# Kernel tuning notes

Measured on AMD Instinct MI355X. Metric: run time of the kernel, lower is better.

The kernel has to match this reference:

```python
import jax, jax.numpy as jnp
import numpy as np

ALPHA = 0.2      # GAT leaky_relu slope (args.alpha)
MLP_SLOPE = 0.01 # F.leaky_relu default in the MLP path
NEG = -9e15

def _l2_normalize(x, axis=1, eps=1e-12):
    n = jnp.sqrt(jnp.sum(x * x, axis=axis, keepdims=True))
    return x / jnp.maximum(n, eps)

def setup_inputs() -> dict:
    key = jax.random.key(0)
    ks = jax.random.split(key, 14)
    N, Din, Dh, H, Dg, M1, M2, E = 8192, 512, 256, 2, 512, 512, 256, 100000
    x = jax.random.normal(ks[0], (N, Din), dtype=jnp.float32)
    adj = jax.random.randint(ks[1], (N, N), 0, 2, dtype=jnp.int32)
    train_sample = jax.random.randint(ks[2], (E, 2), 0, N, dtype=jnp.int32)
    llm_emb = jax.random.normal(ks[3], (N, Dg), dtype=jnp.float32)
    # GAT head params (stacked over heads)
    Wg = jax.random.normal(ks[4], (H, Din, Dh), dtype=jnp.float32) * 0.05
    a1 = jax.random.normal(ks[5], (H, Dh), dtype=jnp.float32) * 0.05
    a2 = jax.random.normal(ks[6], (H, Dh), dtype=jnp.float32) * 0.05
    bias_g = jnp.zeros((H, Dh), dtype=jnp.float32)
    # MLP params
    W1 = jax.random.normal(ks[7], (Dh + Dg, M1), dtype=jnp.float32) * 0.03
    b1 = jnp.zeros((M1,), dtype=jnp.float32)
    W2 = jax.random.normal(ks[8], (M1, M2), dtype=jnp.float32) * 0.04
    b2 = jnp.zeros((M2,), dtype=jnp.float32)
    return {"x": x, "adj": adj, "train_sample": train_sample, "llm_emb": llm_emb,
            "Wg": Wg, "a1": a1, "a2": a2, "bias_g": bias_g,
            "W1": W1, "b1": b1, "W2": W2, "b2": b2}

def reference(x, adj, train_sample, llm_emb, Wg, a1, a2, bias_g, W1, b1, W2, b2):
    mask = adj > 0  # [N, N]

    def head(W, av1, av2, b):
        h = x @ W                                   # [N, Dh]
        s1 = h @ av1                                # [N]
        s2 = h @ av2                                # [N]
        e = jax.nn.leaky_relu(s1[:, None] + s2[None, :], ALPHA)  # [N, N]
        att = jax.nn.softmax(jnp.where(mask, e, NEG), axis=1)
        out = att @ h                               # [N, Dh]
        out = jax.nn.leaky_relu(out, ALPHA)
        out = _l2_normalize(out, axis=1)
        return out + b

    # encode: single GNN layer -> mean over heads (dropout inactive in eval)
    out_heads = jax.vmap(head)(Wg, a1, a2, bias_g)  # [H, N, Dh]
    embed_gnn = jnp.mean(out_heads, axis=0)         # [N, Dh]
    embed = jnp.concatenate([llm_emb, embed_gnn], axis=1)  # [N, Dg+Dh]

    def mlp(z):
        z = jax.nn.leaky_relu(z @ W1 + b1, MLP_SLOPE)
        z = jax.nn.leaky_relu(z @ W2 + b2, MLP_SLOPE)
        return z

    tf_embed = mlp(embed)
    target_embed = mlp(embed)
    train_tf = tf_embed[train_sample[:, 0]]
    train_tg = target_embed[train_sample[:, 1]]
    pred = jnp.sum(train_tf * train_tg, axis=1, keepdims=True)  # dot decode, [E,1]
    return pred
```

## Files before the change

kernel.cpp:

```cpp
#include <hip/hip_runtime.h>
#include <hip/hip_bf16.h>
#include <cstdint>
#include <cstddef>

#define ALPHA 0.2f
#define MLP_SLOPE 0.01f

typedef short bf16x8 __attribute__((ext_vector_type(8)));
typedef float f32x4 __attribute__((ext_vector_type(4)));
typedef unsigned short ushort_t;

#define ASM_BARRIER() __asm__ __volatile__("s_waitcnt lgkmcnt(0)\n\ts_barrier" ::: "memory")

__device__ __forceinline__ float lrelu(float x, float s) { return x > 0.f ? x : x * s; }
__device__ __forceinline__ ushort_t f2bf(float x) {
  __hip_bfloat16 h = __float2bfloat16(x);
  return *reinterpret_cast<ushort_t*>(&h);
}
__device__ __forceinline__ float bf2f(ushort_t u) {
  union { unsigned int i; float f; } v; v.i = ((unsigned int)u) << 16; return v.f;
}

__global__ __launch_bounds__(256) void split_f(
    const float* __restrict__ in, ushort_t* __restrict__ hi,
    ushort_t* __restrict__ lo)
{
  int idx = blockIdx.x * 256 + threadIdx.x;
  float4 v = ((const float4*)in)[idx];
  ushort4 h, l;
  h.x = f2bf(v.x); l.x = f2bf(v.x - bf2f(h.x));
  h.y = f2bf(v.y); l.y = f2bf(v.y - bf2f(h.y));
  h.z = f2bf(v.z); l.z = f2bf(v.z - bf2f(h.z));
  h.w = f2bf(v.w); l.w = f2bf(v.w - bf2f(h.w));
  ((ushort4*)hi)[idx] = h;
  ((ushort4*)lo)[idx] = l;
}

__global__ __launch_bounds__(256) void pack_wt(
    const float* __restrict__ W, ushort_t* __restrict__ hi,
    ushort_t* __restrict__ lo, int K, int N)
{
  int gid = blockIdx.x * 256 + threadIdx.x;
  int lane = gid & 63;
  int kbc = K >> 5;
  int kblk = (gid >> 6) % kbc;
  int nblk = (gid >> 6) / kbc;
  size_t b = (size_t)blockIdx.y * K * N;
  int col = nblk * 16 + (lane & 15);
  int krow = kblk * 32 + (lane >> 4) * 8;
  ushort_t h[8] __attribute__((aligned(16)));
  ushort_t l[8] __attribute__((aligned(16)));
#pragma unroll
  for (int e = 0; e < 8; ++e) {
    float v = W[b + (size_t)(krow + e) * N + col];
    h[e] = f2bf(v);
    l[e] = f2bf(v - bf2f(h[e]));
  }
  *(uint4*)&hi[b + (size_t)gid * 8] = *(uint4*)h;
  *(uint4*)&lo[b + (size_t)gid * 8] = *(uint4*)l;
}

__global__ __launch_bounds__(256) void gemm_nolds(
    const ushort_t* __restrict__ Ahi, const ushort_t* __restrict__ Alo,
    const ushort_t* __restrict__ Bph, const ushort_t* __restrict__ Bpl,
    const float* __restrict__ bias, float* __restrict__ Cf,
    ushort_t* __restrict__ Chi, ushort_t* __restrict__ Clo,
    int M, int N, int K, float slope, int act)
{
  const size_t boff = (size_t)blockIdx.z * N * K;
  const size_t coff = (size_t)blockIdx.z * M * N;
  const int t = threadIdx.x;
  const int wave = t >> 6, l63 = t & 63;
  const int l16 = t & 15, oct = (t >> 4) & 3, quad = oct;
  const int wm = (wave & 1) * 64, wn = (wave >> 1) * 32;
  const int m0 = blockIdx.y * 128 + wm;
  const int nb = blockIdx.x * 4 + (wave >> 1) * 2;
  const int nbase = blockIdx.x * 64 + wn;
  const int ksteps = K >> 5;

  const ushort_t* aph[4];
  const ushort_t* apl[4];
#pragma unroll
  for (int mt = 0; mt < 4; ++mt) {
    size_t o = (size_t)(m0 + mt * 16 + l16) * K + oct * 8;
    aph[mt] = Ahi + o;
    apl[mt] = Alo + o;
  }
  const ushort_t* bph[2];
  const ushort_t* bpl[2];
#pragma unroll
  for (int nt = 0; nt < 2; ++nt) {
    size_t o = boff + ((size_t)(nb + nt) * ksteps * 64 + l63) * 8;
    bph[nt] = Bph + o;
    bpl[nt] = Bpl + o;
  }

  f32x4 acc[4][2];
#pragma unroll
  for (int i = 0; i < 4; ++i)
#pragma unroll
    for (int j = 0; j < 2; ++j) acc[i][j] = (f32x4){0.f, 0.f, 0.f, 0.f};

#define LOADF(AH, AL, BH, BL, KB)                                         \
  {                                                                       \
    _Pragma("unroll") for (int mt = 0; mt < 4; ++mt) {                    \
      AH[mt] = *(const bf16x8*)(aph[mt] + (size_t)(KB) * 32);             \
      AL[mt] = *(const bf16x8*)(apl[mt] + (size_t)(KB) * 32);             \
    }                                                                     \
    _Pragma("unroll") for (int nt = 0; nt < 2; ++nt) {                    \
      BH[nt] = *(const bf16x8*)(bph[nt] + (size_t)(KB) * 512);            \
      BL[nt] = *(const bf16x8*)(bpl[nt] + (size_t)(KB) * 512);            \
    }                                                                     \
  }
#define MF(AH, AL, BH, BL)                                                \
  {                                                                       \
    _Pragma("unroll") for (int mt = 0; mt < 4; ++mt)                      \
    _Pragma("unroll") for (int nt = 0; nt < 2; ++nt) {                    \
      acc[mt][nt] = __builtin_amdgcn_mfma_f32_16x16x32_bf16(AH[mt], BH[nt], acc[mt][nt], 0, 0, 0); \
      acc[mt][nt] = __builtin_amdgcn_mfma_f32_16x16x32_bf16(AH[mt], BL[nt], acc[mt][nt], 0, 0, 0); \
      acc[mt][nt] = __builtin_amdgcn_mfma_f32_16x16x32_bf16(AL[mt], BH[nt], acc[mt][nt], 0, 0, 0); \
    }                                                                     \
  }

  bf16x8 ah0[4], al0[4], bh0[2], bl0[2];
  bf16x8 ah1[4], al1[4], bh1[2], bl1[2];
  LOADF(ah0, al0, bh0, bl0, 0)
  for (int kb = 0; kb < ksteps; kb += 2) {
    LOADF(ah1, al1, bh1, bl1, kb + 1)
    MF(ah0, al0, bh0, bl0)
    if (kb + 2 < ksteps) LOADF(ah0, al0, bh0, bl0, kb + 2)
    MF(ah1, al1, bh1, bl1)
  }
#undef LOADF
#undef MF

#pragma unroll
  for (int mt = 0; mt < 4; ++mt)
#pragma unroll
    for (int nt = 0; nt < 2; ++nt)
#pragma unroll
      for (int rg = 0; rg < 4; ++rg) {
        int m = m0 + mt * 16 + quad * 4 + rg;
        int n = nbase + nt * 16 + l16;
        float v = acc[mt][nt][rg];
        if (bias) v += bias[n];
        if (act) v = lrelu(v, slope);
        size_t o = coff + (size_t)m * N + n;
        if (Cf) Cf[o] = v;
        if (Chi) {
          ushort_t h = f2bf(v);
          Chi[o] = h; Clo[o] = f2bf(v - bf2f(h));
        }
      }
}

__global__ __launch_bounds__(256) void s_kernel(
    const float* __restrict__ hbuf, const float* __restrict__ a1,
    const float* __restrict__ a2, float* __restrict__ s1, float* __restrict__ s2)
{
  const int gw = (blockIdx.x * 256 + threadIdx.x) >> 6;
  const int lane = threadIdx.x & 63;
#pragma unroll
  for (int hh = 0; hh < 2; ++hh) {
    float4 hv = ((const float4*)(hbuf + ((size_t)hh * 8192 + gw) * 256))[lane];
    float4 a1v = ((const float4*)(a1 + hh * 256))[lane];
    float4 a2v = ((const float4*)(a2 + hh * 256))[lane];
    float p1 = hv.x * a1v.x + hv.y * a1v.y + hv.z * a1v.z + hv.w * a1v.w;
    float p2 = hv.x * a2v.x + hv.y * a2v.y + hv.z * a2v.z + hv.w * a2v.w;
    for (int off = 32; off > 0; off >>= 1) {
      p1 += __shfl_xor(p1, off);
      p2 += __shfl_xor(p2, off);
    }
    if (lane == 0) {
      s1[hh * 8192 + gw] = p1;
      s2[hh * 8192 + gw] = p2;
    }
  }
}

__global__ __launch_bounds__(256) void h_pack(
    const float* __restrict__ hbuf, ushort_t* __restrict__ Bpack)
{
  int gid = blockIdx.x * 256 + threadIdx.x;
  int lane = gid & 63;
  int ntile = (gid >> 6) & 15;
  int kblk = (gid >> 10) & 255;
  int head = gid >> 18;
  int c = ntile * 16 + (lane & 15);
  int jb = kblk * 32 + (lane >> 4) * 8;
  ushort_t o[8] __attribute__((aligned(16)));
#pragma unroll
  for (int e = 0; e < 8; ++e)
    o[e] = f2bf(hbuf[((size_t)head * 8192 + jb + e) * 256 + c]);
  *(uint4*)&Bpack[(size_t)gid * 8] = *(uint4*)o;
}

__global__ __launch_bounds__(256, 2) void attn_mfma6(
    const ushort_t* __restrict__ Bpack, const float* __restrict__ s1g,
    const float* __restrict__ s2g, const int* __restrict__ adj,
    ushort_t* __restrict__ pacc, float* __restrict__ pl)
{
  __shared__ ushort_t Wlds[2][2][4][64][8];
  const int t = threadIdx.x;
  const int i0 = blockIdx.x * 64;
  const int js = blockIdx.y;
  const int kbase = js * 2048;
  const int wr = t >> 2, kq = t & 3;
  const int glane = kq * 16 + (wr & 15);
  const int gmt = wr >> 4;
  const float s1v0 = s1g[i0 + wr];
  const float s1v1 = s1g[8192 + i0 + wr];
  const int wave = t >> 6, head = wave >> 1, nh = wave & 1;
  const int l16 = t & 15, quad = (t >> 4) & 3;
  const int l63 = t & 63;
  f32x4 acc[4][8];
#pragma unroll
  for (int m = 0; m < 4; ++m)
#pragma unroll
    for (int n = 0; n < 8; ++n) acc[m][n] = (f32x4){0.f, 0.f, 0.f, 0.f};
  float rs0 = 0.f, rs1 = 0.f;

  const int* arow = adj + (size_t)(i0 + wr) * 8192;
  int4 pa0, pa1;
  float4 p20a, p20b, p21a, p21b;

  auto fetch = [&](int kk) {
    pa0 = *(const int4*)&arow[kk];
    pa1 = *(const int4*)&arow[kk + 4];
    p20a = *(const float4*)&s2g[kk];
    p20b = *(const float4*)&s2g[kk + 4];
    p21a = *(const float4*)&s2g[8192 + kk];
    p21b = *(const float4*)&s2g[8192 + kk + 4];
  };
  auto gen = [&](int buf) {
    int am[8] = {pa0.x, pa0.y, pa0.z, pa0.w, pa1.x, pa1.y, pa1.z, pa1.w};
    float s20[8] = {p20a.x, p20a.y, p20a.z, p20a.w, p20b.x, p20b.y, p20b.z, p20b.w};
    float s21[8] = {p21a.x, p21a.y, p21a.z, p21a.w, p21b.x, p21b.y, p21b.z, p21b.w};
    ushort_t w0[8] __attribute__((aligned(16)));
    ushort_t w1[8] __attribute__((aligned(16)));
#pragma unroll
    for (int e = 0; e < 8; ++e) {
      float e0 = s1v0 + s20[e];
      float e1 = s1v1 + s21[e];
      e0 = fmaxf(e0, 0.f) + ALPHA * fminf(e0, 0.f);
      e1 = fmaxf(e1, 0.f) + ALPHA * fminf(e1, 0.f);
      float v0 = am[e] > 0 ? __expf(e0) : 0.f;
      float v1 = am[e] > 0 ? __expf(e1) : 0.f;
      rs0 += v0; rs1 += v1;
      w0[e] = f2bf(v0); w1[e] = f2bf(v1);
    }
    *(uint4*)&Wlds[buf][0][gmt][glane][0] = *(uint4*)w0;
    *(uint4*)&Wlds[buf][1][gmt][glane][0] = *(uint4*)w1;
  };

  fetch(kbase + kq * 8);
  gen(0);
  fetch(kbase + 32 + kq * 8);
  ASM_BARRIER();

  for (int kt = 0; kt < 64; ++kt) {
    const int cur = kt & 1, nxt = cur ^ 1;
    const int kblk = js * 64 + kt;
    const ushort_t* bb =
        Bpack + ((((size_t)head * 256 + kblk) * 16 + nh * 8) * 64 + l63) * 8;
    bf16x8 Bf[8];
#pragma unroll
    for (int nt = 0; nt < 8; ++nt)
      Bf[nt] = *(const bf16x8*)&bb[nt * 512];
    bf16x8 Af[4];
#pragma unroll
    for (int mt = 0; mt < 4; ++mt)
      Af[mt] = *(const bf16x8*)&Wlds[cur][head][mt][l63][0];
#pragma unroll
    for (int mt = 0; mt < 4; ++mt)
#pragma unroll
      for (int nt = 0; nt < 8; ++nt)
        acc[mt][nt] = __builtin_amdgcn_mfma_f32_16x16x32_bf16(
            Af[mt], Bf[nt], acc[mt][nt], 0, 0, 0);
    if (kt < 63) {
      gen(nxt);
      if (kt < 62) fetch(kbase + (kt + 2) * 32 + kq * 8);
    }
    ASM_BARRIER();
  }

  rs0 += __shfl_xor(rs0, 1); rs0 += __shfl_xor(rs0, 2);
  rs1 += __shfl_xor(rs1, 1); rs1 += __shfl_xor(rs1, 2);
  if (kq == 0) {
    pl[((size_t)js * 2 + 0) * 8192 + i0 + wr] = rs0;
    pl[((size_t)js * 2 + 1) * 8192 + i0 + wr] = rs1;
  }
  const int n0 = nh * 128;
#pragma unroll
  for (int mt = 0; mt < 4; ++mt)
#pragma unroll
    for (int nt = 0; nt < 8; ++nt)
#pragma unroll
      for (int rg = 0; rg < 4; ++rg) {
        int row = i0 + mt * 16 + quad * 4 + rg;
        int col = n0 + nt * 16 + l16;
        pacc[(((size_t)js * 2 + head) * 8192 + row) * 256 + col] =
            f2bf(acc[mt][nt][rg]);
      }
}

__global__ __launch_bounds__(256) void attn_finalize(
    const ushort_t* __restrict__ pacc, const float* __restrict__ pl,
    const float* __restrict__ bg, const float* __restrict__ llm,
    float* __restrict__ embed)
{
  __shared__ float red[8];
  const int r = blockIdx.x;
  const int t = threadIdx.x;
  const int wv = t >> 6, lane = t & 63;
  if (t < 128)
    *(float4*)&embed[(size_t)r * 768 + t * 4] =
        *(const float4*)&llm[(size_t)r * 512 + t * 4];
  float o[2];
#pragma unroll
  for (int hh = 0; hh < 2; ++hh) {
    float num = 0.f, l = 0.f;
#pragma unroll
    for (int js = 0; js < 4; ++js) {
      num += bf2f(pacc[(((size_t)js * 2 + hh) * 8192 + r) * 256 + t]);
      l += pl[((size_t)js * 2 + hh) * 8192 + r];
    }
    o[hh] = lrelu(num / l, ALPHA);
  }
  float v0 = o[0] * o[0], v1 = o[1] * o[1];
  for (int off = 32; off > 0; off >>= 1) {
    v0 += __shfl_xor(v0, off);
    v1 += __shfl_xor(v1, off);
  }
  if (lane == 0) { red[wv] = v0; red[4 + wv] = v1; }
  __syncthreads();
  float n0 = fmaxf(sqrtf(red[0] + red[1] + red[2] + red[3]), 1e-12f);
  float n1 = fmaxf(sqrtf(red[4] + red[5] + red[6] + red[7]), 1e-12f);
  embed[(size_t)r * 768 + 512 + t] =
      0.5f * (o[0] / n0 + bg[t] + o[1] / n1 + bg[256 + t]);
}

__global__ __launch_bounds__(256) void pred_kernel(
    const float* __restrict__ z2, const int* __restrict__ ts,
    float* __restrict__ out, int E)
{
  const int gw = (blockIdx.x * 256 + threadIdx.x) >> 6;
  const int lane = threadIdx.x & 63;
  if (gw >= E) return;
  const int a = ts[gw * 2], b = ts[gw * 2 + 1];
  float4 va = ((const float4*)(z2 + (size_t)a * 256))[lane];
  float4 vb = ((const float4*)(z2 + (size_t)b * 256))[lane];
  float p = va.x * vb.x + va.y * vb.y + va.z * vb.z + va.w * vb.w;
  for (int off = 32; off > 0; off >>= 1) p += __shfl_xor(p, off);
  if (lane == 0) out[gw] = p;
}

extern "C" void kernel_launch(void* const* d_in, const int* in_sizes, int n_in,
                              void* d_out, int out_size, void* d_ws, size_t ws_size,
                              hipStream_t stream) {
  const float* x   = (const float*)d_in[0];
  const int*   adj = (const int*)d_in[1];
  const int*   ts  = (const int*)d_in[2];
  const float* llm = (const float*)d_in[3];
  const float* Wg  = (const float*)d_in[4];
  const float* a1  = (const float*)d_in[5];
  const float* a2  = (const float*)d_in[6];
  const float* bg  = (const float*)d_in[7];
  const float* W1  = (const float*)d_in[8];
  const float* b1  = (const float*)d_in[9];
  const float* W2  = (const float*)d_in[10];
  const float* b2  = (const float*)d_in[11];
  float* out = (float*)d_out;
  float* ws  = (float*)d_ws;
  const int E = in_sizes[2] / 2;

  float*    hbuf  = ws;
  ushort_t* Bpack = (ushort_t*)(ws + 4194304);
  float*    embed = ws;
  ushort_t* xhi   = (ushort_t*)(ws + 6291456);
  ushort_t* xlo   = (ushort_t*)(ws + 8388608);
  ushort_t* z1hi  = xhi;
  ushort_t* z1lo  = xlo;
  float*    s1    = ws + 10485760;
  float*    s2    = ws + 10502144;
  float*    pl    = ws + 10518528;
  ushort_t* pacc  = (ushort_t*)(ws + 10584064);
  ushort_t* ehi   = (ushort_t*)(ws + 10584064);
  ushort_t* elo   = (ushort_t*)(ws + 13729792);
  float*    z2    = ws + 16875520;
  ushort_t* wgphi = (ushort_t*)(ws + 18972672);
  ushort_t* wgplo = (ushort_t*)(ws + 19103744);
  ushort_t* w1phi = (ushort_t*)(ws + 19234816);
  ushort_t* w1plo = (ushort_t*)(ws + 19431424);
  ushort_t* w2phi = (ushort_t*)(ws + 19628032);
  ushort_t* w2plo = (ushort_t*)(ws + 19693568);

  split_f<<<4096, 256, 0, stream>>>(x, xhi, xlo);
  pack_wt<<<dim3(64, 2), 256, 0, stream>>>(Wg, wgphi, wgplo, 512, 256);
  pack_wt<<<dim3(192, 1), 256, 0, stream>>>(W1, w1phi, w1plo, 768, 512);
  pack_wt<<<dim3(64, 1), 256, 0, stream>>>(W2, w2phi, w2plo, 512, 256);
  gemm_nolds<<<dim3(4, 64, 2), 256, 0, stream>>>(
      xhi, xlo, wgphi, wgplo, nullptr, hbuf, nullptr, nullptr,
      8192, 256, 512, 0.f, 0);
  s_kernel<<<2048, 256, 0, stream>>>(hbuf, a1, a2, s1, s2);
  h_pack<<<2048, 256, 0, stream>>>(hbuf, Bpack);
  attn_mfma6<<<dim3(128, 4), 256, 0, stream>>>(Bpack, s1, s2, adj, pacc, pl);
  attn_finalize<<<8192, 256, 0, stream>>>(pacc, pl, bg, llm, embed);
  split_f<<<6144, 256, 0, stream>>>(embed, ehi, elo);
  gemm_nolds<<<dim3(8, 64, 1), 256, 0, stream>>>(
      ehi, elo, w1phi, w1plo, b1, nullptr, z1hi, z1lo,
      8192, 512, 768, MLP_SLOPE, 1);
  gemm_nolds<<<dim3(4, 64, 1), 256, 0, stream>>>(
      z1hi, z1lo, w2phi, w2plo, b2, z2, nullptr, nullptr,
      8192, 256, 512, MLP_SLOPE, 1);
  pred_kernel<<<(E * 64 + 255) / 256, 256, 0, stream>>>(z2, ts, out, E);
}
```

Baseline: 658.7 us.

## Shrink attention row tile to 32 rows and split heads across threads

The attention kernel now processes 32 query rows per block instead of 64, doubling the grid. The weight-generation work is split so each thread handles one head instead of both, and launch bounds rise to 3 blocks per SM. This cuts accumulator registers and per-thread exp work to raise occupancy and parallelism. The cost is that each Bpack tile is loaded for half as many rows, doubling B-operand global traffic per output and lowering the MFMA-to-load ratio.

Result: slower. 750.7 us (+14.0%).

```diff
diff --git a/kernel.cpp b/kernel.cpp
--- a/kernel.cpp
+++ b/kernel.cpp
@@ -195,62 +195,56 @@
   *(uint4*)&Bpack[(size_t)gid * 8] = *(uint4*)o;
 }
 
-__global__ __launch_bounds__(256, 2) void attn_mfma6(
+__global__ __launch_bounds__(256, 3) void attn_mfma7(
     const ushort_t* __restrict__ Bpack, const float* __restrict__ s1g,
     const float* __restrict__ s2g, const int* __restrict__ adj,
     ushort_t* __restrict__ pacc, float* __restrict__ pl)
 {
-  __shared__ ushort_t Wlds[2][2][4][64][8];
+  __shared__ ushort_t Wlds[2][2][2][64][8];
   const int t = threadIdx.x;
-  const int i0 = blockIdx.x * 64;
+  const int i0 = blockIdx.x * 32;
   const int js = blockIdx.y;
   const int kbase = js * 2048;
-  const int wr = t >> 2, kq = t & 3;
+  const int wr = t >> 3;
+  const int ghead = (t >> 2) & 1;
+  const int kq = t & 3;
   const int glane = kq * 16 + (wr & 15);
   const int gmt = wr >> 4;
-  const float s1v0 = s1g[i0 + wr];
-  const float s1v1 = s1g[8192 + i0 + wr];
+  const float s1v = s1g[(size_t)ghead * 8192 + i0 + wr];
+  const float* s2h = s2g + (size_t)ghead * 8192;
+  const int* arow = adj + (size_t)(i0 + wr) * 8192;
   const int wave = t >> 6, head = wave >> 1, nh = wave & 1;
   const int l16 = t & 15, quad = (t >> 4) & 3;
   const int l63 = t & 63;
-  f32x4 acc[4][8];
-#pragma unroll
-  for (int m = 0; m < 4; ++m)
+  f32x4 acc[2][8];
+#pragma unroll
+  for (int m = 0; m < 2; ++m)
 #pragma unroll
     for (int n = 0; n < 8; ++n) acc[m][n] = (f32x4){0.f, 0.f, 0.f, 0.f};
-  float rs0 = 0.f, rs1 = 0.f;
-
-  const int* arow = adj + (size_t)(i0 + wr) * 8192;
+  float rs = 0.f;
+
   int4 pa0, pa1;
-  float4 p20a, p20b, p21a, p21b;
-
+  float4 ps2a, ps2b;
   auto fetch = [&](int kk) {
     pa0 = *(const int4*)&arow[kk];
     pa1 = *(const int4*)&arow[kk + 4];
-    p20a = *(const float4*)&s2g[kk];
-    p20b = *(const float4*)&s2g[kk + 4];
-    p21a = *(const float4*)&s2g[8192 + kk];
-    p21b = *(const float4*)&s2g[8192 + kk + 4];
+    ps2a = *(const float4*)&s2h[kk];
+    ps2b = *(const float4*)&s2h[kk + 4];
   };
   auto gen = [&](int buf) {
     int am[8] = {pa0.x, pa0.y, pa0.z, pa0.w, pa1.x, pa1.y, pa1.z, pa1.w};
-    float s20[8] = {p20a.x, p20a.y, p20a.z, p20a.w, p20b.x, p20b.y, p20b.z, p20b.w};
-    float s21[8] = {p21a.x, p21a.y, p21a.z, p21a.w, p21b.x, p21b.y, p21b.z, p21b.w};
-    ushort_t w0[8] __attribute__((aligned(16)));
-    ushort_t w1[8] __attribute__((aligned(16)));
+    float s2v[8] = {ps2a.x, ps2a.y, ps2a.z, ps2a.w,
+                    ps2b.x, ps2b.y, ps2b.z, ps2b.w};
+    ushort_t w[8] __attribute__((aligned(16)));
 #pragma unroll
     for (int e = 0; e < 8; ++e) {
-      float e0 = s1v0 + s20[e];
-      float e1 = s1v1 + s21[e];
-      e0 = fmaxf(e0, 0.f) + ALPHA * fminf(e0, 0.f);
-      e1 = fmaxf(e1, 0.f) + ALPHA * fminf(e1, 0.f);
-      float v0 = am[e] > 0 ? __expf(e0) : 0.f;
-      float v1 = am[e] > 0 ? __expf(e1) : 0.f;
-      rs0 += v0; rs1 += v1;
-      w0[e] = f2bf(v0); w1[e] = f2bf(v1);
+      float ev = s1v + s2v[e];
+      ev = fmaxf(ev, 0.f) + ALPHA * fminf(ev, 0.f);
+      float wv = am[e] > 0 ? __expf(ev) : 0.f;
+      rs += wv;
+      w[e] = f2bf(wv);
     }
-    *(uint4*)&Wlds[buf][0][gmt][glane][0] = *(uint4*)w0;
-    *(uint4*)&Wlds[buf][1][gmt][glane][0] = *(uint4*)w1;
+    *(uint4*)&Wlds[buf][ghead][gmt][glane][0] = *(uint4*)w;
   };
 
   fetch(kbase + kq * 8);
@@ -267,12 +261,12 @@
 #pragma unroll
     for (int nt = 0; nt < 8; ++nt)
       Bf[nt] = *(const bf16x8*)&bb[nt * 512];
-    bf16x8 Af[4];
-#pragma unroll
-    for (int mt = 0; mt < 4; ++mt)
+    bf16x8 Af[2];
+#pragma unroll
+    for (int mt = 0; mt < 2; ++mt)
       Af[mt] = *(const bf16x8*)&Wlds[cur][head][mt][l63][0];
 #pragma unroll
-    for (int mt = 0; mt < 4; ++mt)
+    for (int mt = 0; mt < 2; ++mt)
 #pragma unroll
       for (int nt = 0; nt < 8; ++nt)
         acc[mt][nt] = __builtin_amdgcn_mfma_f32_16x16x32_bf16(
@@ -284,15 +278,13 @@
     ASM_BARRIER();
   }
 
-  rs0 += __shfl_xor(rs0, 1); rs0 += __shfl_xor(rs0, 2);
-  rs1 += __shfl_xor(rs1, 1); rs1 += __shfl_xor(rs1, 2);
-  if (kq == 0) {
-    pl[((size_t)js * 2 + 0) * 8192 + i0 + wr] = rs0;
-    pl[((size_t)js * 2 + 1) * 8192 + i0 + wr] = rs1;
-  }
+  rs += __shfl_xor(rs, 1); rs += __shfl_xor(rs, 2);
+  if (kq == 0)
+    pl[((size_t)js * 2 + ghead) * 8192 + i0 + wr] = rs;
+
   const int n0 = nh * 128;
 #pragma unroll
-  for (int mt = 0; mt < 4; ++mt)
+  for (int mt = 0; mt < 2; ++mt)
 #pragma unroll
     for (int nt = 0; nt < 8; ++nt)
 #pragma unroll
@@ -404,7 +396,7 @@
       8192, 256, 512, 0.f, 0);
   s_kernel<<<2048, 256, 0, stream>>>(hbuf, a1, a2, s1, s2);
   h_pack<<<2048, 256, 0, stream>>>(hbuf, Bpack);
-  attn_mfma6<<<dim3(128, 4), 256, 0, stream>>>(Bpack, s1, s2, adj, pacc, pl);
+  attn_mfma7<<<dim3(256, 4), 256, 0, stream>>>(Bpack, s1, s2, adj, pacc, pl);
   attn_finalize<<<8192, 256, 0, stream>>>(pacc, pl, bg, llm, embed);
   split_f<<<6144, 256, 0, stream>>>(embed, ehi, elo);
   gemm_nolds<<<dim3(8, 64, 1), 256, 0, stream>>>(
```

## Fuse GAT projection with score/pack epilogue, single-bf16 x, LDS-staged GEMMs

Applied to the files above, without the earlier changes.

The x@Wg projection now uses a single bf16 pass instead of the hi/lo split. Its epilogue writes the packed bf16 B-operand for attention directly and accumulates s1/s2 with atomics, which removes the fp32 hbuf round trip and the separate s_kernel and h_pack launches. attn_finalize writes the split bf16 embedding directly, so the separate split pass is gone. The MLP GEMMs stage A tiles through double-buffered LDS. Dropping the lo term for x and h lowers precision, and the atomics make the s1/s2 summation order nondeterministic.

Result: faster. 594.5 us (-9.8%).

```diff
diff --git a/kernel.cpp b/kernel.cpp
--- a/kernel.cpp
+++ b/kernel.cpp
@@ -21,19 +21,20 @@
   union { unsigned int i; float f; } v; v.i = ((unsigned int)u) << 16; return v.f;
 }
 
-__global__ __launch_bounds__(256) void split_f(
-    const float* __restrict__ in, ushort_t* __restrict__ hi,
-    ushort_t* __restrict__ lo)
+__global__ __launch_bounds__(256) void tobf(
+    const float* __restrict__ in, ushort_t* __restrict__ outp)
 {
   int idx = blockIdx.x * 256 + threadIdx.x;
   float4 v = ((const float4*)in)[idx];
-  ushort4 h, l;
-  h.x = f2bf(v.x); l.x = f2bf(v.x - bf2f(h.x));
-  h.y = f2bf(v.y); l.y = f2bf(v.y - bf2f(h.y));
-  h.z = f2bf(v.z); l.z = f2bf(v.z - bf2f(h.z));
-  h.w = f2bf(v.w); l.w = f2bf(v.w - bf2f(h.w));
-  ((ushort4*)hi)[idx] = h;
-  ((ushort4*)lo)[idx] = l;
+  ushort4 h;
+  h.x = f2bf(v.x); h.y = f2bf(v.y); h.z = f2bf(v.z); h.w = f2bf(v.w);
+  ((ushort4*)outp)[idx] = h;
+}
+
+__global__ __launch_bounds__(256) void zero_f(float* __restrict__ p)
+{
+  int idx = blockIdx.x * 256 + threadIdx.x;
+  ((float4*)p)[idx] = make_float4(0.f, 0.f, 0.f, 0.f);
 }
 
 __global__ __launch_bounds__(256) void pack_wt(
@@ -57,43 +58,127 @@
     l[e] = f2bf(v - bf2f(h[e]));
   }
   *(uint4*)&hi[b + (size_t)gid * 8] = *(uint4*)h;
-  *(uint4*)&lo[b + (size_t)gid * 8] = *(uint4*)l;
-}
-
-__global__ __launch_bounds__(256) void gemm_nolds(
+  if (lo) *(uint4*)&lo[b + (size_t)gid * 8] = *(uint4*)l;
+}
+
+__global__ __launch_bounds__(256, 2) void gemm_h(
+    const ushort_t* __restrict__ xb, const ushort_t* __restrict__ Wgp,
+    const float* __restrict__ a1, const float* __restrict__ a2,
+    ushort_t* __restrict__ Bpack, float* __restrict__ s1,
+    float* __restrict__ s2)
+{
+  __shared__ ushort_t Ab[2][128][40];
+  const int t = threadIdx.x;
+  const int head = blockIdx.z;
+  const int m0 = blockIdx.y * 128;
+  const int n0 = blockIdx.x * 64;
+  const int wave = t >> 6;
+  const int wm = (wave & 1) * 64, wn = (wave >> 1) * 32;
+  const int l16 = t & 15, quad = (t >> 4) & 3, l63 = t & 63;
+  const int sr = t >> 1, sp = (t & 1) * 16;
+  const ushort_t* arow_g = xb + (size_t)(m0 + sr) * 512 + sp;
+  const ushort_t* bp = Wgp + (size_t)head * 256 * 512;
+  const int nb0 = (n0 + wn) >> 4;
+
+  f32x4 acc[4][2];
+#pragma unroll
+  for (int i = 0; i < 4; ++i)
+#pragma unroll
+    for (int j = 0; j < 2; ++j) acc[i][j] = (f32x4){0.f, 0.f, 0.f, 0.f};
+
+  uint4 r0, r1;
+  r0 = *(const uint4*)(arow_g);
+  r1 = *(const uint4*)(arow_g + 8);
+  *(uint4*)&Ab[0][sr][sp] = r0;
+  *(uint4*)&Ab[0][sr][sp + 8] = r1;
+  __syncthreads();
+
+  for (int kb = 0; kb < 16; ++kb) {
+    const int cur = kb & 1, nxt = cur ^ 1;
+    if (kb < 15) {
+      const ushort_t* p = arow_g + (kb + 1) * 32;
+      r0 = *(const uint4*)p;
+      r1 = *(const uint4*)(p + 8);
+    }
+    bf16x8 Bf[2];
+#pragma unroll
+    for (int nt = 0; nt < 2; ++nt)
+      Bf[nt] = *(const bf16x8*)&bp[(((size_t)(nb0 + nt) * 16 + kb) * 64 + l63) * 8];
+    bf16x8 Af[4];
+#pragma unroll
+    for (int mt = 0; mt < 4; ++mt)
+      Af[mt] = *(const bf16x8*)&Ab[cur][wm + mt * 16 + l16][quad * 8];
+#pragma unroll
+    for (int mt = 0; mt < 4; ++mt)
+#pragma unroll
+      for (int nt = 0; nt < 2; ++nt)
+        acc[mt][nt] = __builtin_amdgcn_mfma_f32_16x16x32_bf16(
+            Af[mt], Bf[nt], acc[mt][nt], 0, 0, 0);
+    if (kb < 15) {
+      *(uint4*)&Ab[nxt][sr][sp] = r0;
+      *(uint4*)&Ab[nxt][sr][sp + 8] = r1;
+    }
+    __syncthreads();
+  }
+
+#pragma unroll
+  for (int mt = 0; mt < 4; ++mt)
+#pragma unroll
+    for (int nt = 0; nt < 2; ++nt)
+#pragma unroll
+      for (int rg = 0; rg < 4; ++rg) {
+        int j = m0 + wm + mt * 16 + quad * 4 + rg;
+        int c = n0 + wn + nt * 16 + l16;
+        int kblk = j >> 5;
+        int laneb = ((j >> 3) & 3) * 16 + (c & 15);
+        int e = j & 7;
+        Bpack[(((size_t)head * 256 + kblk) * 16 + (c >> 4)) * 512 + laneb * 8 + e] =
+            f2bf(acc[mt][nt][rg]);
+      }
+  float a1v[2], a2v[2];
+#pragma unroll
+  for (int nt = 0; nt < 2; ++nt) {
+    int c = n0 + wn + nt * 16 + l16;
+    a1v[nt] = a1[head * 256 + c];
+    a2v[nt] = a2[head * 256 + c];
+  }
+#pragma unroll
+  for (int mt = 0; mt < 4; ++mt)
+#pragma unroll
+    for (int rg = 0; rg < 4; ++rg) {
+      float p1 = acc[mt][0][rg] * a1v[0] + acc[mt][1][rg] * a1v[1];
+      float p2 = acc[mt][0][rg] * a2v[0] + acc[mt][1][rg] * a2v[1];
+      p1 += __shfl_xor(p1, 1); p2 += __shfl_xor(p2, 1);
+      p1 += __shfl_xor(p1, 2); p2 += __shfl_xor(p2, 2);
+      p1 += __shfl_xor(p1, 4); p2 += __shfl_xor(p2, 4);
+      p1 += __shfl_xor(p1, 8); p2 += __shfl_xor(p2, 8);
+      if (l16 == 0) {
+        int row = m0 + wm + mt * 16 + quad * 4 + rg;
+        atomicAdd(&s1[head * 8192 + row], p1);
+        atomicAdd(&s2[head * 8192 + row], p2);
+      }
+    }
+}
+
+__global__ __launch_bounds__(256, 2) void gemm_mlp(
     const ushort_t* __restrict__ Ahi, const ushort_t* __restrict__ Alo,
     const ushort_t* __restrict__ Bph, const ushort_t* __restrict__ Bpl,
     const float* __restrict__ bias, float* __restrict__ Cf,
     ushort_t* __restrict__ Chi, ushort_t* __restrict__ Clo,
-    int M, int N, int K, float slope, int act)
-{
-  const size_t boff = (size_t)blockIdx.z * N * K;
-  const size_t coff = (size_t)blockIdx.z * M * N;
+    int M, int N, int K, float slope)
+{
+  __shared__ ushort_t Ah[2][128][40], Al[2][128][40];
+  const int kbc = K >> 5;
   const int t = threadIdx.x;
-  const int wave = t >> 6, l63 = t & 63;
-  const int l16 = t & 15, oct = (t >> 4) & 3, quad = oct;
+  const int m0 = blockIdx.y * 128;
+  const int n0 = blockIdx.x * 64;
+  const int wave = t >> 6;
   const int wm = (wave & 1) * 64, wn = (wave >> 1) * 32;
-  const int m0 = blockIdx.y * 128 + wm;
-  const int nb = blockIdx.x * 4 + (wave >> 1) * 2;
-  const int nbase = blockIdx.x * 64 + wn;
-  const int ksteps = K >> 5;
-
-  const ushort_t* aph[4];
-  const ushort_t* apl[4];
-#pragma unroll
-  for (int mt = 0; mt < 4; ++mt) {
-    size_t o = (size_t)(m0 + mt * 16 + l16) * K + oct * 8;
-    aph[mt] = Ahi + o;
-    apl[mt] = Alo + o;
-  }
-  const ushort_t* bph[2];
-  const ushort_t* bpl[2];
-#pragma unroll
-  for (int nt = 0; nt < 2; ++nt) {
-    size_t o = boff + ((size_t)(nb + nt) * ksteps * 64 + l63) * 8;
-    bph[nt] = Bph + o;
-    bpl[nt] = Bpl + o;
-  }
+  const int l16 = t & 15, quad = (t >> 4) & 3, l63 = t & 63;
+  const int sr = t >> 1, sp = (t & 1) * 16;
+  const ushort_t* ah_g = Ahi + (size_t)(m0 + sr) * K + sp;
+  const ushort_t* al_g = Alo + (size_t)(m0 + sr) * K + sp;
+  const int nb0 = (n0 + wn) >> 4;
 
   f32x4 acc[4][2];
 #pragma unroll
@@ -101,38 +186,56 @@
 #pragma unroll
     for (int j = 0; j < 2; ++j) acc[i][j] = (f32x4){0.f, 0.f, 0.f, 0.f};
 
-#define LOADF(AH, AL, BH, BL, KB)                                         \
-  {                                                                       \
-    _Pragma("unroll") for (int mt = 0; mt < 4; ++mt) {                    \
-      AH[mt] = *(const bf16x8*)(aph[mt] + (size_t)(KB) * 32);             \
-      AL[mt] = *(const bf16x8*)(apl[mt] + (size_t)(KB) * 32);             \
-    }                                                                     \
-    _Pragma("unroll") for (int nt = 0; nt < 2; ++nt) {                    \
-      BH[nt] = *(const bf16x8*)(bph[nt] + (size_t)(KB) * 512);            \
-      BL[nt] = *(const bf16x8*)(bpl[nt] + (size_t)(KB) * 512);            \
-    }                                                                     \
-  }
-#define MF(AH, AL, BH, BL)                                                \
-  {                                                                       \
-    _Pragma("unroll") for (int mt = 0; mt < 4; ++mt)                      \
-    _Pragma("unroll") for (int nt = 0; nt < 2; ++nt) {                    \
-      acc[mt][nt] = __builtin_amdgcn_mfma_f32_16x16x32_bf16(AH[mt], BH[nt], acc[mt][nt], 0, 0, 0); \
-      acc[mt][nt] = __builtin_amdgcn_mfma_f32_16x16x32_bf16(AH[mt], BL[nt], acc[mt][nt], 0, 0, 0); \
-      acc[mt][nt] = __builtin_amdgcn_mfma_f32_16x16x32_bf16(AL[mt], BH[nt], acc[mt][nt], 0, 0, 0); \
-    }                                                                     \
-  }
-
-  bf16x8 ah0[4], al0[4], bh0[2], bl0[2];
-  bf16x8 ah1[4], al1[4], bh1[2], bl1[2];
-  LOADF(ah0, al0, bh0, bl0, 0)
-  for (int kb = 0; kb < ksteps; kb += 2) {
-    LOADF(ah1, al1, bh1, bl1, kb + 1)
-    MF(ah0, al0, bh0, bl0)
-    if (kb + 2 < ksteps) LOADF(ah0, al0, bh0, bl0, kb + 2)
-    MF(ah1, al1, bh1, bl1)
-  }
-#undef LOADF
-#undef MF
+  uint4 rh0, rh1, rl0, rl1;
+  rh0 = *(const uint4*)(ah_g);
+  rh1 = *(const uint4*)(ah_g + 8);
+  rl0 = *(const uint4*)(al_g);
+  rl1 = *(const uint4*)(al_g + 8);
+  *(uint4*)&Ah[0][sr][sp] = rh0;
+  *(uint4*)&Ah[0][sr][sp + 8] = rh1;
+  *(uint4*)&Al[0][sr][sp] = rl0;
+  *(uint4*)&Al[0][sr][sp + 8] = rl1;
+  __syncthreads();
+
+  for (int kb = 0; kb < kbc; ++kb) {
+    const int cur = kb & 1, nxt = cur ^ 1;
+    if (kb + 1 < kbc) {
+      const ushort_t* ph = ah_g + (kb + 1) * 32;
+      const ushort_t* plo = al_g + (kb + 1) * 32;
+      rh0 = *(const uint4*)ph;
+      rh1 = *(const uint4*)(ph + 8);
+      rl0 = *(const uint4*)plo;
+      rl1 = *(const uint4*)(plo + 8);
+    }
+    bf16x8 bh[2], bl[2];
+#pragma unroll
+    for (int nt = 0; nt < 2; ++nt) {
+      size_t o = (((size_t)(nb0 + nt) * kbc + kb) * 64 + l63) * 8;
+      bh[nt] = *(const bf16x8*)&Bph[o];
+      bl[nt] = *(const bf16x8*)&Bpl[o];
+    }
+    bf16x8 afh[4], afl[4];
+#pragma unroll
+    for (int mt = 0; mt < 4; ++mt) {
+      afh[mt] = *(const bf16x8*)&Ah[cur][wm + mt * 16 + l16][quad * 8];
+      afl[mt] = *(const bf16x8*)&Al[cur][wm + mt * 16 + l16][quad * 8];
+    }
+#pragma unroll
+    for (int mt = 0; mt < 4; ++mt)
+#pragma unroll
+      for (int nt = 0; nt < 2; ++nt) {
+        acc[mt][nt] = __builtin_amdgcn_mfma_f32_16x16x32_bf16(afh[mt], bh[nt], acc[mt][nt], 0, 0, 0);
+        acc[mt][nt] = __builtin_amdgcn_mfma_f32_16x16x32_bf16(afh[mt], bl[nt], acc[mt][nt], 0, 0, 0);
+        acc[mt][nt] = __builtin_amdgcn_mfma_f32_16x16x32_bf16(afl[mt], bh[nt], acc[mt][nt], 0, 0, 0);
+      }
+    if (kb + 1 < kbc) {
+      *(uint4*)&Ah[nxt][sr][sp] = rh0;
+      *(uint4*)&Ah[nxt][sr][sp + 8] = rh1;
+      *(uint4*)&Al[nxt][sr][sp] = rl0;
+      *(uint4*)&Al[nxt][sr][sp + 8] = rl1;
+    }
+    __syncthreads();
+  }
 
 #pragma unroll
   for (int mt = 0; mt < 4; ++mt)
@@ -140,59 +243,16 @@
     for (int nt = 0; nt < 2; ++nt)
 #pragma unroll
       for (int rg = 0; rg < 4; ++rg) {
-        int m = m0 + mt * 16 + quad * 4 + rg;
-        int n = nbase + nt * 16 + l16;
-        float v = acc[mt][nt][rg];
-        if (bias) v += bias[n];
-        if (act) v = lrelu(v, slope);
-        size_t o = coff + (size_t)m * N + n;
+        int m = m0 + wm + mt * 16 + quad * 4 + rg;
+        int n = n0 + wn + nt * 16 + l16;
+        float v = lrelu(acc[mt][nt][rg] + bias[n], slope);
+        size_t o = (size_t)m * N + n;
         if (Cf) Cf[o] = v;
         if (Chi) {
           ushort_t h = f2bf(v);
           Chi[o] = h; Clo[o] = f2bf(v - bf2f(h));
         }
       }
-}
-
-__global__ __launch_bounds__(256) void s_kernel(
-    const float* __restrict__ hbuf, const float* __restrict__ a1,
-    const float* __restrict__ a2, float* __restrict__ s1, float* __restrict__ s2)
-{
-  const int gw = (blockIdx.x * 256 + threadIdx.x) >> 6;
-  const int lane = threadIdx.x & 63;
-#pragma unroll
-  for (int hh = 0; hh < 2; ++hh) {
-    float4 hv = ((const float4*)(hbuf + ((size_t)hh * 8192 + gw) * 256))[lane];
-    float4 a1v = ((const float4*)(a1 + hh * 256))[lane];
-    float4 a2v = ((const float4*)(a2 + hh * 256))[lane];
-    float p1 = hv.x * a1v.x + hv.y * a1v.y + hv.z * a1v.z + hv.w * a1v.w;
-    float p2 = hv.x * a2v.x + hv.y * a2v.y + hv.z * a2v.z + hv.w * a2v.w;
-    for (int off = 32; off > 0; off >>= 1) {
-      p1 += __shfl_xor(p1, off);
-      p2 += __shfl_xor(p2, off);
-    }
-    if (lane == 0) {
-      s1[hh * 8192 + gw] = p1;
-      s2[hh * 8192 + gw] = p2;
-    }
-  }
-}
-
-__global__ __launch_bounds__(256) void h_pack(
-    const float* __restrict__ hbuf, ushort_t* __restrict__ Bpack)
-{
-  int gid = blockIdx.x * 256 + threadIdx.x;
-  int lane = gid & 63;
-  int ntile = (gid >> 6) & 15;
-  int kblk = (gid >> 10) & 255;
-  int head = gid >> 18;
-  int c = ntile * 16 + (lane & 15);
-  int jb = kblk * 32 + (lane >> 4) * 8;
-  ushort_t o[8] __attribute__((aligned(16)));
-#pragma unroll
-  for (int e = 0; e < 8; ++e)
-    o[e] = f2bf(hbuf[((size_t)head * 8192 + jb + e) * 256 + c]);
-  *(uint4*)&Bpack[(size_t)gid * 8] = *(uint4*)o;
 }
 
 __global__ __launch_bounds__(256, 2) void attn_mfma6(
@@ -307,15 +367,19 @@
 __global__ __launch_bounds__(256) void attn_finalize(
     const ushort_t* __restrict__ pacc, const float* __restrict__ pl,
     const float* __restrict__ bg, const float* __restrict__ llm,
-    float* __restrict__ embed)
+    ushort_t* __restrict__ ehi, ushort_t* __restrict__ elo)
 {
   __shared__ float red[8];
   const int r = blockIdx.x;
   const int t = threadIdx.x;
   const int wv = t >> 6, lane = t & 63;
-  if (t < 128)
-    *(float4*)&embed[(size_t)r * 768 + t * 4] =
-        *(const float4*)&llm[(size_t)r * 512 + t * 4];
+#pragma unroll
+  for (int half = 0; half < 2; ++half) {
+    float lv = llm[(size_t)r * 512 + half * 256 + t];
+    ushort_t h = f2bf(lv);
+    ehi[(size_t)r * 768 + half * 256 + t] = h;
+    elo[(size_t)r * 768 + half * 256 + t] = f2bf(lv - bf2f(h));
+  }
   float o[2];
 #pragma unroll
   for (int hh = 0; hh < 2; ++hh) {
@@ -336,8 +400,10 @@
   __syncthreads();
   float n0 = fmaxf(sqrtf(red[0] + red[1] + red[2] + red[3]), 1e-12f);
   float n1 = fmaxf(sqrtf(red[4] + red[5] + red[6] + red[7]), 1e-12f);
-  embed[(size_t)r * 768 + 512 + t] =
-      0.5f * (o[0] / n0 + bg[t] + o[1] / n1 + bg[256 + t]);
+  float val = 0.5f * (o[0] / n0 + bg[t] + o[1] / n1 + bg[256 + t]);
+  ushort_t h = f2bf(val);
+  ehi[(size_t)r * 768 + 512 + t] = h;
+  elo[(size_t)r * 768 + 512 + t] = f2bf(val - bf2f(h));
 }
 
 __global__ __launch_bounds__(256) void pred_kernel(
@@ -374,44 +440,34 @@
   float* ws  = (float*)d_ws;
   const int E = in_sizes[2] / 2;
 
-  float*    hbuf  = ws;
-  ushort_t* Bpack = (ushort_t*)(ws + 4194304);
-  float*    embed = ws;
-  ushort_t* xhi   = (ushort_t*)(ws + 6291456);
-  ushort_t* xlo   = (ushort_t*)(ws + 8388608);
-  ushort_t* z1hi  = xhi;
-  ushort_t* z1lo  = xlo;
-  float*    s1    = ws + 10485760;
-  float*    s2    = ws + 10502144;
-  float*    pl    = ws + 10518528;
-  ushort_t* pacc  = (ushort_t*)(ws + 10584064);
-  ushort_t* ehi   = (ushort_t*)(ws + 10584064);
-  ushort_t* elo   = (ushort_t*)(ws + 13729792);
-  float*    z2    = ws + 16875520;
-  ushort_t* wgphi = (ushort_t*)(ws + 18972672);
-  ushort_t* wgplo = (ushort_t*)(ws + 19103744);
-  ushort_t* w1phi = (ushort_t*)(ws + 19234816);
-  ushort_t* w1plo = (ushort_t*)(ws + 19431424);
-  ushort_t* w2phi = (ushort_t*)(ws + 19628032);
-  ushort_t* w2plo = (ushort_t*)(ws + 19693568);
-
-  split_f<<<4096, 256, 0, stream>>>(x, xhi, xlo);
-  pack_wt<<<dim3(64, 2), 256, 0, stream>>>(Wg, wgphi, wgplo, 512, 256);
-  pack_wt<<<dim3(192, 1), 256, 0, stream>>>(W1, w1phi, w1plo, 768, 512);
-  pack_wt<<<dim3(64, 1), 256, 0, stream>>>(W2, w2phi, w2plo, 512, 256);
-  gemm_nolds<<<dim3(4, 64, 2), 256, 0, stream>>>(
-      xhi, xlo, wgphi, wgplo, nullptr, hbuf, nullptr, nullptr,
-      8192, 256, 512, 0.f, 0);
-  s_kernel<<<2048, 256, 0, stream>>>(hbuf, a1, a2, s1, s2);
-  h_pack<<<2048, 256, 0, stream>>>(hbuf, Bpack);
+  ushort_t* xb    = (ushort_t*)(ws + 0);
+  ushort_t* Wgp   = (ushort_t*)(ws + 2097152);
+  ushort_t* W1ph  = (ushort_t*)(ws + 2228224);
+  ushort_t* W1pl  = (ushort_t*)(ws + 2424832);
+  ushort_t* W2ph  = (ushort_t*)(ws + 2621440);
+  ushort_t* W2pl  = (ushort_t*)(ws + 2686976);
+  ushort_t* Bpack = (ushort_t*)(ws + 2752512);
+  float*    s1    = ws + 4849664;
+  float*    s2    = ws + 4866048;
+  float*    pl    = ws + 4882432;
+  ushort_t* pacc  = (ushort_t*)(ws + 4947968);
+  ushort_t* ehi   = (ushort_t*)(ws + 13336576);
+  ushort_t* elo   = (ushort_t*)(ws + 16482304);
+  ushort_t* z1hi  = (ushort_t*)(ws + 19628032);
+  ushort_t* z1lo  = (ushort_t*)(ws + 21725184);
+  float*    z2    = ws + 23822336;
+
+  tobf<<<4096, 256, 0, stream>>>(x, xb);
+  pack_wt<<<dim3(64, 2), 256, 0, stream>>>(Wg, Wgp, nullptr, 512, 256);
+  pack_wt<<<dim3(192, 1), 256, 0, stream>>>(W1, W1ph, W1pl, 768, 512);
+  pack_wt<<<dim3(64, 1), 256, 0, stream>>>(W2, W2ph, W2pl, 512, 256);
+  zero_f<<<32, 256, 0, stream>>>(s1);
+  gemm_h<<<dim3(4, 64, 2), 256, 0, stream>>>(xb, Wgp, a1, a2, Bpack, s1, s2);
   attn_mfma6<<<dim3(128, 4), 256, 0, stream>>>(Bpack, s1, s2, adj, pacc, pl);
-  attn_finalize<<<8192, 256, 0, stream>>>(pacc, pl, bg, llm, embed);
-  split_f<<<6144, 256, 0, stream>>>(embed, ehi, elo);
-  gemm_nolds<<<dim3(8, 64, 1), 256, 0, stream>>>(
-      ehi, elo, w1phi, w1plo, b1, nullptr, z1hi, z1lo,
-      8192, 512, 768, MLP_SLOPE, 1);
-  gemm_nolds<<<dim3(4, 64, 1), 256, 0, stream>>>(
-      z1hi, z1lo, w2phi, w2plo, b2, z2, nullptr, nullptr,
-      8192, 256, 512, MLP_SLOPE, 1);
+  attn_finalize<<<8192, 256, 0, stream>>>(pacc, pl, bg, llm, ehi, elo);
+  gemm_mlp<<<dim3(8, 64), 256, 0, stream>>>(
+      ehi, elo, W1ph, W1pl, b1, nullptr, z1hi, z1lo, 8192, 512, 768, MLP_SLOPE);
+  gemm_mlp<<<dim3(4, 64), 256, 0, stream>>>(
+      z1hi, z1lo, W2ph, W2pl, b2, z2, nullptr, nullptr, 8192, 256, 512, MLP_SLOPE);
   pred_kernel<<<(E * 64 + 255) / 256, 256, 0, stream>>>(z2, ts, out, E);
 }
```
